# Kernel optimization log

Measured on AMD Instinct MI355X. Metric: run time of the kernel, lower is better.

## Reference

```python
import jax, jax.numpy as jnp
import numpy as np

B = 8192
COND_DIM = 64
OUT_DIM = 64      # output_dim (joint velocity dim)
ACT_DIM = 8       # action_dim (latent action dim)
H1, H2 = 256, 256


def setup_inputs() -> dict:
    key = jax.random.key(0)
    ks = jax.random.split(key, 8)
    inp = {
        "cond_inp": jax.random.normal(ks[0], (B, COND_DIM), dtype=jnp.float32),
        "low_level_action": jax.random.normal(ks[1], (B, OUT_DIM), dtype=jnp.float32),
        # MLP params: cond_dim -> 256 -> 256 -> action_dim*output_dim
        "W1": jax.random.normal(ks[2], (COND_DIM, H1), dtype=jnp.float32) / np.sqrt(COND_DIM),
        "b1": jnp.zeros((H1,), dtype=jnp.float32),
        "W2": jax.random.normal(ks[3], (H1, H2), dtype=jnp.float32) / np.sqrt(H1),
        "b2": jnp.zeros((H2,), dtype=jnp.float32),
        "W3": jax.random.normal(ks[4], (H2, ACT_DIM * OUT_DIM), dtype=jnp.float32) / np.sqrt(H2),
        "b3": jnp.zeros((ACT_DIM * OUT_DIM,), dtype=jnp.float32),
    }
    return inp


def _householder(Hcols):
    # Hcols: [B, n, k]; chain of k batched Householder reflections.
    n = Hcols.shape[1]
    k = Hcols.shape[2]
    I = jnp.eye(n, dtype=Hcols.dtype)
    Q = jnp.broadcast_to(I, (Hcols.shape[0], n, n))
    for c in range(k):  # small fixed unroll over latent action columns
        v = Hcols[:, :, c]                                  # [B, n]
        vvT = jnp.einsum('bi,bj->bij', v, v)                # [B, n, n]
        vTv = jnp.einsum('bi,bi->b', v, v)[:, None, None]   # [B, 1, 1]
        Qi = I - 2.0 * vvT / vTv
        Q = jnp.matmul(Qi, Q)
    return Q[:, :, :k]


def reference(cond_inp, low_level_action, W1, b1, W2, b2, W3, b3):
    # MLP h(cond_inp)
    x = jnp.tanh(cond_inp @ W1 + b1)
    x = jnp.tanh(x @ W2 + b2)
    x = x @ W3 + b3                                    # [B, act*out]
    Hcols = x.reshape(-1, OUT_DIM, ACT_DIM)            # [B, out, act]
    scl_map = _householder(Hcols)                      # [B, out, act], orthonormal cols
    # best action: a* = S^T qdot ; reconstruction: qdot_hat = S a*
    a_star = jnp.einsum('bnk,bn->bk', scl_map, low_level_action)   # [B, act]
    q_dot_hat = jnp.einsum('bnk,bk->bn', scl_map, a_star)          # [B, out]
    return q_dot_hat[..., None]                        # [B, out, 1] (matches tf.matmul shape)
```

## Files before the change

### kernel.cpp

```cpp
#include <hip/hip_runtime.h>

typedef float f4 __attribute__((ext_vector_type(4)));
typedef float f32x4 __attribute__((ext_vector_type(4)));
typedef _Float16 f16x8 __attribute__((ext_vector_type(8)));

#define HSWZ16(o) ((o) ^ (((o) >> 3) & 0x70))

#define BARLG() asm volatile("s_waitcnt lgkmcnt(0)\n\ts_barrier" ::: "memory")

__global__ __launch_bounds__(256) void prep_frags_all(
    const float* __restrict__ W1, const float* __restrict__ W2,
    const float* __restrict__ W3, _Float16* __restrict__ dst) {
    __shared__ float s[32 * 264];
    const int b = blockIdx.x, tid = threadIdx.x;
    const float* W; int N, kt, nh, KT; size_t off;
    if (b < 2)       { W = W1; N = 256; KT = 2; kt = b;            nh = 0;          off = 0; }
    else if (b < 10) { W = W2; N = 256; KT = 8; kt = b - 2;        nh = 0;          off = 16384; }
    else             { W = W3; N = 512; KT = 8; kt = (b - 10) >> 1; nh = (b - 10) & 1; off = 81920; }
    #pragma unroll
    for (int rep = 0; rep < 8; ++rep) {
        int fi = rep * 256 + tid;
        int row = fi >> 6, c4 = fi & 63;
        f4 v = *(const f4*)&W[(kt * 32 + row) * N + nh * 256 + c4 * 4];
        *(f4*)&s[row * 264 + c4 * 4] = v;
    }
    __syncthreads();
    const int wv = tid >> 6, l = tid & 63, lr = l & 15, lg = l >> 4;
    #pragma unroll
    for (int p = 0; p < 4; ++p) {
        int lnt = wv * 4 + p;
        f16x8 o;
        #pragma unroll
        for (int j = 0; j < 8; ++j)
            o[j] = (_Float16)s[(lg * 8 + j) * 264 + lnt * 16 + lr];
        int page = (nh * 16 + lnt) * KT + kt;
        *(f16x8*)&dst[off + (size_t)page * 512 + l * 8] = o;
    }
}

__device__ __forceinline__ float ftanh(float x) {
    float e = __expf(2.0f * x);
    return 1.0f - 2.0f / (e + 1.0f);
}
__device__ __forceinline__ float red8(float x) {
    x += __shfl_xor(x, 1); x += __shfl_xor(x, 2); x += __shfl_xor(x, 4);
    return x;
}

__global__ __launch_bounds__(1024, 4) void scl_mfma(
    const float* __restrict__ cond, const float* __restrict__ act,
    const float* __restrict__ b1, const float* __restrict__ b2,
    const float* __restrict__ b3,
    const _Float16* __restrict__ wf,
    float* __restrict__ out)
{
    __shared__ char smem[33792];
    _Float16* x1 = (_Float16*)smem;
    _Float16* x2 = (_Float16*)(smem + 16896);

    const int tid = threadIdx.x;
    const int w   = tid >> 6;
    const int l   = tid & 63;
    const int lr  = l & 15;
    const int lg  = l >> 4;
    const int rb  = blockIdx.x * 32;
    const f16x8* wp = (const f16x8*)wf;

    f16x8 a1[2][2];
    #pragma unroll
    for (int m = 0; m < 2; ++m) {
        const float* crow = cond + (rb + m * 16 + lr) * 64 + lg * 8;
        #pragma unroll
        for (int kt = 0; kt < 2; ++kt) {
            f4 va = *(const f4*)(crow + kt * 32);
            f4 vb = *(const f4*)(crow + kt * 32 + 4);
            #pragma unroll
            for (int j = 0; j < 4; ++j) {
                a1[m][kt][j]     = (_Float16)va[j];
                a1[m][kt][4 + j] = (_Float16)vb[j];
            }
        }
    }
    f16x8 w1f[2];
    #pragma unroll
    for (int kt = 0; kt < 2; ++kt) w1f[kt] = wp[(w * 2 + kt) * 64 + l];
    f16x8 w2f[8];
    #pragma unroll
    for (int kt = 0; kt < 8; ++kt) w2f[kt] = wp[2048 + (w * 8 + kt) * 64 + l];
    float b1v = b1[w * 16 + lr];
    float b2v = b2[w * 16 + lr];
    float b3v[2];
    #pragma unroll
    for (int n = 0; n < 2; ++n) b3v[n] = b3[(w * 2 + n) * 16 + lr];

    f4 av0 = {}, av1 = {};
    if (w < 4) {
        const float* ap = act + (rb + w * 8 + (l >> 3)) * 64 + (l & 7) * 8;
        av0 = *(const f4*)ap;
        av1 = *(const f4*)(ap + 4);
    }

    {
        f32x4 acc[2] = {};
        #pragma unroll
        for (int kt = 0; kt < 2; ++kt)
            #pragma unroll
            for (int m = 0; m < 2; ++m)
                acc[m] = __builtin_amdgcn_mfma_f32_16x16x32_f16(a1[m][kt], w1f[kt], acc[m], 0, 0, 0);
        #pragma unroll
        for (int m = 0; m < 2; ++m)
            #pragma unroll
            for (int r = 0; r < 4; ++r) {
                float v = ftanh(acc[m][r] + b1v);
                x1[(m * 16 + lg * 4 + r) * 264 + w * 16 + lr] = (_Float16)v;
            }
    }
    BARLG();

    f16x8 w3a[2][4];
    #pragma unroll
    for (int n = 0; n < 2; ++n)
        #pragma unroll
        for (int kt = 0; kt < 4; ++kt)
            w3a[n][kt] = wp[10240 + ((w * 2 + n) * 8 + kt) * 64 + l];
    {
        f32x4 acc[2] = {};
        #pragma unroll
        for (int kt = 0; kt < 8; ++kt) {
            int cb = kt * 32 + lg * 8;
            f16x8 am0 = *(const f16x8*)&x1[lr * 264 + cb];
            f16x8 am1 = *(const f16x8*)&x1[(16 + lr) * 264 + cb];
            acc[0] = __builtin_amdgcn_mfma_f32_16x16x32_f16(am0, w2f[kt], acc[0], 0, 0, 0);
            acc[1] = __builtin_amdgcn_mfma_f32_16x16x32_f16(am1, w2f[kt], acc[1], 0, 0, 0);
        }
        #pragma unroll
        for (int m = 0; m < 2; ++m)
            #pragma unroll
            for (int r = 0; r < 4; ++r) {
                float v = ftanh(acc[m][r] + b2v);
                x2[(m * 16 + lg * 4 + r) * 264 + w * 16 + lr] = (_Float16)v;
            }
    }
    BARLG();

    f16x8 w3b[2][4];
    #pragma unroll
    for (int n = 0; n < 2; ++n)
        #pragma unroll
        for (int kt = 0; kt < 4; ++kt)
            w3b[n][kt] = wp[10240 + ((w * 2 + n) * 8 + (kt + 4)) * 64 + l];
    f32x4 acc3[2][2] = {};
    #pragma unroll
    for (int kt = 0; kt < 4; ++kt) {
        int cb = kt * 32 + lg * 8;
        f16x8 am0 = *(const f16x8*)&x2[lr * 264 + cb];
        f16x8 am1 = *(const f16x8*)&x2[(16 + lr) * 264 + cb];
        #pragma unroll
        for (int n = 0; n < 2; ++n) {
            acc3[0][n] = __builtin_amdgcn_mfma_f32_16x16x32_f16(am0, w3a[n][kt], acc3[0][n], 0, 0, 0);
            acc3[1][n] = __builtin_amdgcn_mfma_f32_16x16x32_f16(am1, w3a[n][kt], acc3[1][n], 0, 0, 0);
        }
    }
    #pragma unroll
    for (int kt = 4; kt < 8; ++kt) {
        int cb = kt * 32 + lg * 8;
        f16x8 am0 = *(const f16x8*)&x2[lr * 264 + cb];
        f16x8 am1 = *(const f16x8*)&x2[(16 + lr) * 264 + cb];
        #pragma unroll
        for (int n = 0; n < 2; ++n) {
            acc3[0][n] = __builtin_amdgcn_mfma_f32_16x16x32_f16(am0, w3b[n][kt - 4], acc3[0][n], 0, 0, 0);
            acc3[1][n] = __builtin_amdgcn_mfma_f32_16x16x32_f16(am1, w3b[n][kt - 4], acc3[1][n], 0, 0, 0);
        }
    }
    BARLG();

    #pragma unroll
    for (int n = 0; n < 2; ++n) {
        int col = (w * 2 + n) * 16 + lr;
        #pragma unroll
        for (int m = 0; m < 2; ++m)
            #pragma unroll
            for (int r = 0; r < 4; ++r) {
                int row = m * 16 + lg * 4 + r;
                *(_Float16*)(smem + row * 1056 + HSWZ16(col * 2)) =
                    (_Float16)(acc3[m][n][r] + b3v[n]);
            }
    }
    BARLG();

    if (w < 4) {
        const int c = l & 7;
        const int hrow = w * 8 + (l >> 3);
        const int grow = rb + hrow;
        f16x8 hv[8];
        #pragma unroll
        for (int j = 0; j < 8; ++j)
            hv[j] = *(const f16x8*)(smem + hrow * 1056 + HSWZ16((c * 8 + j) * 16));
        float h[8][8];
        #pragma unroll
        for (int cc = 0; cc < 8; ++cc)
            #pragma unroll
            for (int j = 0; j < 8; ++j)
                h[cc][j] = (float)hv[j][cc];
        float inv[8];
        #pragma unroll
        for (int cc = 0; cc < 8; ++cc) {
            float s = 0.0f;
            #pragma unroll
            for (int j = 0; j < 8; ++j) s += h[cc][j] * h[cc][j];
            inv[cc] = 2.0f / red8(s);
        }
        float u[8] = {av0[0], av0[1], av0[2], av0[3], av1[0], av1[1], av1[2], av1[3]};
        #pragma unroll
        for (int cc = 7; cc >= 0; --cc) {
            float d = 0.0f;
            #pragma unroll
            for (int j = 0; j < 8; ++j) d += h[cc][j] * u[j];
            float t = inv[cc] * red8(d);
            #pragma unroll
            for (int j = 0; j < 8; ++j) u[j] -= t * h[cc][j];
        }
        float wv[8];
        #pragma unroll
        for (int j = 0; j < 8; ++j) wv[j] = (c == 0) ? u[j] : 0.0f;
        #pragma unroll
        for (int cc = 0; cc < 8; ++cc) {
            float d = 0.0f;
            #pragma unroll
            for (int j = 0; j < 8; ++j) d += h[cc][j] * wv[j];
            float t = inv[cc] * red8(d);
            #pragma unroll
            for (int j = 0; j < 8; ++j) wv[j] -= t * h[cc][j];
        }
        f4 o0 = {wv[0], wv[1], wv[2], wv[3]};
        f4 o1 = {wv[4], wv[5], wv[6], wv[7]};
        float* op = out + grow * 64 + c * 8;
        *(f4*)op = o0;
        *(f4*)(op + 4) = o1;
    }
}

extern "C" void kernel_launch(void* const* d_in, const int* in_sizes, int n_in,
                              void* d_out, int out_size, void* d_ws, size_t ws_size,
                              hipStream_t stream) {
    const float* cond = (const float*)d_in[0];
    const float* act  = (const float*)d_in[1];
    const float* W1   = (const float*)d_in[2];
    const float* b1   = (const float*)d_in[3];
    const float* W2   = (const float*)d_in[4];
    const float* b2   = (const float*)d_in[5];
    const float* W3   = (const float*)d_in[6];
    const float* b3   = (const float*)d_in[7];
    float* outp = (float*)d_out;

    _Float16* wf = (_Float16*)d_ws;
    prep_frags_all<<<dim3(26), dim3(256), 0, stream>>>(W1, W2, W3, wf);
    scl_mfma<<<dim3(256), dim3(1024), 0, stream>>>(cond, act, b1, b2, b3, wf, outp);
}
```

Measured before the change: 25.51 us.

## Restructure MLP into single-wave blocks computing transposed GEMMs over all output tiles

Replaces the 1024-thread, 32-row blocks with 64-thread single-wave blocks that each handle 16 rows. Every wave loops over all output column tiles, with weights as the A operand and activations as the B operand, and folds the bias into the accumulator init. Hidden activations round-trip through swizzled LDS private to the wave, so no barriers are needed. This removes block-wide synchronization and the idle waves in the Householder phase. In exchange, each wave streams the full weight set from global/L2 and only 512 waves run, which may leave the machine underoccupied and bound on weight bandwidth.

```diff
diff --git a/kernel.cpp b/kernel.cpp
--- a/kernel.cpp
+++ b/kernel.cpp
@@ -3,10 +3,14 @@
 typedef float f4 __attribute__((ext_vector_type(4)));
 typedef float f32x4 __attribute__((ext_vector_type(4)));
 typedef _Float16 f16x8 __attribute__((ext_vector_type(8)));
-
-#define HSWZ16(o) ((o) ^ (((o) >> 3) & 0x70))
-
-#define BARLG() asm volatile("s_waitcnt lgkmcnt(0)\n\ts_barrier" ::: "memory")
+typedef _Float16 f16x4 __attribute__((ext_vector_type(4)));
+
+__device__ __forceinline__ int XSW(int row, int fb) {
+    return row * 512 + (fb ^ ((row & 7) << 4));
+}
+__device__ __forceinline__ int HBY(int row, int k, int sub) {
+    return row * 1024 + (((k ^ ((k >> 3) & 7) ^ (row & 7)) << 4) + sub);
+}
 
 __global__ __launch_bounds__(256) void prep_frags_all(
     const float* __restrict__ W1, const float* __restrict__ W2,
@@ -47,155 +51,96 @@
     return x;
 }
 
-__global__ __launch_bounds__(1024, 4) void scl_mfma(
+__global__ __launch_bounds__(64, 2) void scl_wave(
     const float* __restrict__ cond, const float* __restrict__ act,
     const float* __restrict__ b1, const float* __restrict__ b2,
     const float* __restrict__ b3,
     const _Float16* __restrict__ wf,
     float* __restrict__ out)
 {
-    __shared__ char smem[33792];
-    _Float16* x1 = (_Float16*)smem;
-    _Float16* x2 = (_Float16*)(smem + 16896);
-
-    const int tid = threadIdx.x;
-    const int w   = tid >> 6;
-    const int l   = tid & 63;
-    const int lr  = l & 15;
-    const int lg  = l >> 4;
-    const int rb  = blockIdx.x * 32;
+    __shared__ char smem[16384];
+
+    const int l  = threadIdx.x;
+    const int lr = l & 15, lg = l >> 4;
+    const int rb = blockIdx.x * 16;
     const f16x8* wp = (const f16x8*)wf;
 
-    f16x8 a1[2][2];
-    #pragma unroll
-    for (int m = 0; m < 2; ++m) {
-        const float* crow = cond + (rb + m * 16 + lr) * 64 + lg * 8;
+    f4 av[2][2];
+    #pragma unroll
+    for (int p = 0; p < 2; ++p) {
+        const float* ap = act + (rb + 8 * p + (l >> 3)) * 64 + (l & 7) * 8;
+        av[p][0] = *(const f4*)ap;
+        av[p][1] = *(const f4*)(ap + 4);
+    }
+    f16x8 bc[2];
+    {
+        const float* crow = cond + (rb + lr) * 64 + lg * 8;
         #pragma unroll
         for (int kt = 0; kt < 2; ++kt) {
             f4 va = *(const f4*)(crow + kt * 32);
             f4 vb = *(const f4*)(crow + kt * 32 + 4);
             #pragma unroll
             for (int j = 0; j < 4; ++j) {
-                a1[m][kt][j]     = (_Float16)va[j];
-                a1[m][kt][4 + j] = (_Float16)vb[j];
+                bc[kt][j]     = (_Float16)va[j];
+                bc[kt][4 + j] = (_Float16)vb[j];
             }
         }
     }
-    f16x8 w1f[2];
-    #pragma unroll
-    for (int kt = 0; kt < 2; ++kt) w1f[kt] = wp[(w * 2 + kt) * 64 + l];
-    f16x8 w2f[8];
-    #pragma unroll
-    for (int kt = 0; kt < 8; ++kt) w2f[kt] = wp[2048 + (w * 8 + kt) * 64 + l];
-    float b1v = b1[w * 16 + lr];
-    float b2v = b2[w * 16 + lr];
-    float b3v[2];
-    #pragma unroll
-    for (int n = 0; n < 2; ++n) b3v[n] = b3[(w * 2 + n) * 16 + lr];
-
-    f4 av0 = {}, av1 = {};
-    if (w < 4) {
-        const float* ap = act + (rb + w * 8 + (l >> 3)) * 64 + (l & 7) * 8;
-        av0 = *(const f4*)ap;
-        av1 = *(const f4*)(ap + 4);
-    }
-
-    {
-        f32x4 acc[2] = {};
+
+    #pragma unroll 4
+    for (int nt = 0; nt < 16; ++nt) {
+        f4 bi = *(const f4*)&b1[nt * 16 + lg * 4];
+        f32x4 acc = {bi[0], bi[1], bi[2], bi[3]};
         #pragma unroll
         for (int kt = 0; kt < 2; ++kt)
-            #pragma unroll
-            for (int m = 0; m < 2; ++m)
-                acc[m] = __builtin_amdgcn_mfma_f32_16x16x32_f16(a1[m][kt], w1f[kt], acc[m], 0, 0, 0);
-        #pragma unroll
-        for (int m = 0; m < 2; ++m)
-            #pragma unroll
-            for (int r = 0; r < 4; ++r) {
-                float v = ftanh(acc[m][r] + b1v);
-                x1[(m * 16 + lg * 4 + r) * 264 + w * 16 + lr] = (_Float16)v;
-            }
-    }
-    BARLG();
-
-    f16x8 w3a[2][4];
-    #pragma unroll
-    for (int n = 0; n < 2; ++n)
-        #pragma unroll
-        for (int kt = 0; kt < 4; ++kt)
-            w3a[n][kt] = wp[10240 + ((w * 2 + n) * 8 + kt) * 64 + l];
-    {
-        f32x4 acc[2] = {};
-        #pragma unroll
-        for (int kt = 0; kt < 8; ++kt) {
-            int cb = kt * 32 + lg * 8;
-            f16x8 am0 = *(const f16x8*)&x1[lr * 264 + cb];
-            f16x8 am1 = *(const f16x8*)&x1[(16 + lr) * 264 + cb];
-            acc[0] = __builtin_amdgcn_mfma_f32_16x16x32_f16(am0, w2f[kt], acc[0], 0, 0, 0);
-            acc[1] = __builtin_amdgcn_mfma_f32_16x16x32_f16(am1, w2f[kt], acc[1], 0, 0, 0);
-        }
-        #pragma unroll
-        for (int m = 0; m < 2; ++m)
-            #pragma unroll
-            for (int r = 0; r < 4; ++r) {
-                float v = ftanh(acc[m][r] + b2v);
-                x2[(m * 16 + lg * 4 + r) * 264 + w * 16 + lr] = (_Float16)v;
-            }
-    }
-    BARLG();
-
-    f16x8 w3b[2][4];
-    #pragma unroll
-    for (int n = 0; n < 2; ++n)
-        #pragma unroll
-        for (int kt = 0; kt < 4; ++kt)
-            w3b[n][kt] = wp[10240 + ((w * 2 + n) * 8 + (kt + 4)) * 64 + l];
-    f32x4 acc3[2][2] = {};
-    #pragma unroll
-    for (int kt = 0; kt < 4; ++kt) {
-        int cb = kt * 32 + lg * 8;
-        f16x8 am0 = *(const f16x8*)&x2[lr * 264 + cb];
-        f16x8 am1 = *(const f16x8*)&x2[(16 + lr) * 264 + cb];
-        #pragma unroll
-        for (int n = 0; n < 2; ++n) {
-            acc3[0][n] = __builtin_amdgcn_mfma_f32_16x16x32_f16(am0, w3a[n][kt], acc3[0][n], 0, 0, 0);
-            acc3[1][n] = __builtin_amdgcn_mfma_f32_16x16x32_f16(am1, w3a[n][kt], acc3[1][n], 0, 0, 0);
-        }
-    }
-    #pragma unroll
-    for (int kt = 4; kt < 8; ++kt) {
-        int cb = kt * 32 + lg * 8;
-        f16x8 am0 = *(const f16x8*)&x2[lr * 264 + cb];
-        f16x8 am1 = *(const f16x8*)&x2[(16 + lr) * 264 + cb];
-        #pragma unroll
-        for (int n = 0; n < 2; ++n) {
-            acc3[0][n] = __builtin_amdgcn_mfma_f32_16x16x32_f16(am0, w3b[n][kt - 4], acc3[0][n], 0, 0, 0);
-            acc3[1][n] = __builtin_amdgcn_mfma_f32_16x16x32_f16(am1, w3b[n][kt - 4], acc3[1][n], 0, 0, 0);
-        }
-    }
-    BARLG();
-
-    #pragma unroll
-    for (int n = 0; n < 2; ++n) {
-        int col = (w * 2 + n) * 16 + lr;
-        #pragma unroll
-        for (int m = 0; m < 2; ++m)
-            #pragma unroll
-            for (int r = 0; r < 4; ++r) {
-                int row = m * 16 + lg * 4 + r;
-                *(_Float16*)(smem + row * 1056 + HSWZ16(col * 2)) =
-                    (_Float16)(acc3[m][n][r] + b3v[n]);
-            }
-    }
-    BARLG();
-
-    if (w < 4) {
-        const int c = l & 7;
-        const int hrow = w * 8 + (l >> 3);
-        const int grow = rb + hrow;
+            acc = __builtin_amdgcn_mfma_f32_16x16x32_f16(wp[(nt * 2 + kt) * 64 + l], bc[kt], acc, 0, 0, 0);
+        f16x4 hp;
+        #pragma unroll
+        for (int r = 0; r < 4; ++r) hp[r] = (_Float16)ftanh(acc[r]);
+        *(f16x4*)(smem + XSW(lr, (nt * 16 + lg * 4) * 2)) = hp;
+    }
+
+    f16x8 xf[8];
+    #pragma unroll
+    for (int kt = 0; kt < 8; ++kt)
+        xf[kt] = *(const f16x8*)(smem + XSW(lr, (kt * 32 + lg * 8) * 2));
+    #pragma unroll 2
+    for (int nt = 0; nt < 16; ++nt) {
+        f4 bi = *(const f4*)&b2[nt * 16 + lg * 4];
+        f32x4 acc = {bi[0], bi[1], bi[2], bi[3]};
+        #pragma unroll
+        for (int kt = 0; kt < 8; ++kt)
+            acc = __builtin_amdgcn_mfma_f32_16x16x32_f16(wp[2048 + (nt * 8 + kt) * 64 + l], xf[kt], acc, 0, 0, 0);
+        f16x4 hp;
+        #pragma unroll
+        for (int r = 0; r < 4; ++r) hp[r] = (_Float16)ftanh(acc[r]);
+        *(f16x4*)(smem + XSW(lr, (nt * 16 + lg * 4) * 2)) = hp;
+    }
+
+    f16x8 yf[8];
+    #pragma unroll
+    for (int kt = 0; kt < 8; ++kt)
+        yf[kt] = *(const f16x8*)(smem + XSW(lr, (kt * 32 + lg * 8) * 2));
+    #pragma unroll 2
+    for (int nt = 0; nt < 32; ++nt) {
+        f4 bi = *(const f4*)&b3[nt * 16 + lg * 4];
+        f32x4 acc = {bi[0], bi[1], bi[2], bi[3]};
+        #pragma unroll
+        for (int kt = 0; kt < 8; ++kt)
+            acc = __builtin_amdgcn_mfma_f32_16x16x32_f16(wp[10240 + (nt * 8 + kt) * 64 + l], yf[kt], acc, 0, 0, 0);
+        f16x4 hp;
+        #pragma unroll
+        for (int r = 0; r < 4; ++r) hp[r] = (_Float16)acc[r];
+        *(f16x4*)(smem + HBY(lr, 2 * nt + (lg >> 1), 8 * (lg & 1))) = hp;
+    }
+
+    #pragma unroll
+    for (int p = 0; p < 2; ++p) {
+        const int c = l & 7, br = 8 * p + (l >> 3);
         f16x8 hv[8];
         #pragma unroll
         for (int j = 0; j < 8; ++j)
-            hv[j] = *(const f16x8*)(smem + hrow * 1056 + HSWZ16((c * 8 + j) * 16));
+            hv[j] = *(const f16x8*)(smem + HBY(br, 8 * c + j, 0));
         float h[8][8];
         #pragma unroll
         for (int cc = 0; cc < 8; ++cc)
@@ -210,7 +155,8 @@
             for (int j = 0; j < 8; ++j) s += h[cc][j] * h[cc][j];
             inv[cc] = 2.0f / red8(s);
         }
-        float u[8] = {av0[0], av0[1], av0[2], av0[3], av1[0], av1[1], av1[2], av1[3]};
+        float u[8] = {av[p][0][0], av[p][0][1], av[p][0][2], av[p][0][3],
+                      av[p][1][0], av[p][1][1], av[p][1][2], av[p][1][3]};
         #pragma unroll
         for (int cc = 7; cc >= 0; --cc) {
             float d = 0.0f;
@@ -232,9 +178,9 @@
             #pragma unroll
             for (int j = 0; j < 8; ++j) wv[j] -= t * h[cc][j];
         }
+        float* op = out + (rb + br) * 64 + c * 8;
         f4 o0 = {wv[0], wv[1], wv[2], wv[3]};
         f4 o1 = {wv[4], wv[5], wv[6], wv[7]};
-        float* op = out + grow * 64 + c * 8;
         *(f4*)op = o0;
         *(f4*)(op + 4) = o1;
     }
@@ -255,5 +201,5 @@
 
     _Float16* wf = (_Float16*)d_ws;
     prep_frags_all<<<dim3(26), dim3(256), 0, stream>>>(W1, W2, W3, wf);
-    scl_mfma<<<dim3(256), dim3(1024), 0, stream>>>(cond, act, b1, b2, b3, wf, outp);
-}
+    scl_wave<<<dim3(512), dim3(64), 0, stream>>>(cond, act, b1, b2, b3, wf, outp);
+}
```

After: 62.07 us. 2.43x slower.

## Drop weight-prep kernel; load fp32 weight fragments directly in main kernel

Applied to the files above, without the earlier changes.

Removes the separate prep kernel that converted the weights to fp16 MFMA fragment layout. The main kernel now gathers and converts fragments straight from the fp32 weight matrices using strided scalar loads. The point is to save one kernel launch and its serial dependency. The cost is that 256 blocks each do uncoalesced strided fp32 loads, which multiplies weight traffic, though that traffic is mostly L2-resident. Biases are also folded into the accumulator initial values instead of being added after the MFMAs.

```diff
diff --git a/kernel.cpp b/kernel.cpp
--- a/kernel.cpp
+++ b/kernel.cpp
@@ -1,42 +1,13 @@
 #include <hip/hip_runtime.h>
 
 typedef float f4 __attribute__((ext_vector_type(4)));
+typedef float f2 __attribute__((ext_vector_type(2)));
 typedef float f32x4 __attribute__((ext_vector_type(4)));
 typedef _Float16 f16x8 __attribute__((ext_vector_type(8)));
 
 #define HSWZ16(o) ((o) ^ (((o) >> 3) & 0x70))
 
 #define BARLG() asm volatile("s_waitcnt lgkmcnt(0)\n\ts_barrier" ::: "memory")
-
-__global__ __launch_bounds__(256) void prep_frags_all(
-    const float* __restrict__ W1, const float* __restrict__ W2,
-    const float* __restrict__ W3, _Float16* __restrict__ dst) {
-    __shared__ float s[32 * 264];
-    const int b = blockIdx.x, tid = threadIdx.x;
-    const float* W; int N, kt, nh, KT; size_t off;
-    if (b < 2)       { W = W1; N = 256; KT = 2; kt = b;            nh = 0;          off = 0; }
-    else if (b < 10) { W = W2; N = 256; KT = 8; kt = b - 2;        nh = 0;          off = 16384; }
-    else             { W = W3; N = 512; KT = 8; kt = (b - 10) >> 1; nh = (b - 10) & 1; off = 81920; }
-    #pragma unroll
-    for (int rep = 0; rep < 8; ++rep) {
-        int fi = rep * 256 + tid;
-        int row = fi >> 6, c4 = fi & 63;
-        f4 v = *(const f4*)&W[(kt * 32 + row) * N + nh * 256 + c4 * 4];
-        *(f4*)&s[row * 264 + c4 * 4] = v;
-    }
-    __syncthreads();
-    const int wv = tid >> 6, l = tid & 63, lr = l & 15, lg = l >> 4;
-    #pragma unroll
-    for (int p = 0; p < 4; ++p) {
-        int lnt = wv * 4 + p;
-        f16x8 o;
-        #pragma unroll
-        for (int j = 0; j < 8; ++j)
-            o[j] = (_Float16)s[(lg * 8 + j) * 264 + lnt * 16 + lr];
-        int page = (nh * 16 + lnt) * KT + kt;
-        *(f16x8*)&dst[off + (size_t)page * 512 + l * 8] = o;
-    }
-}
 
 __device__ __forceinline__ float ftanh(float x) {
     float e = __expf(2.0f * x);
@@ -47,11 +18,21 @@
     return x;
 }
 
+template<int N>
+__device__ __forceinline__ f16x8 ldfrag(const float* __restrict__ W,
+                                        int kt, int nt, int l) {
+    const float* p = W + (size_t)(kt * 32 + ((l >> 4) << 3)) * N + nt * 16 + (l & 15);
+    f16x8 o;
+    #pragma unroll
+    for (int j = 0; j < 8; ++j) o[j] = (_Float16)p[j * N];
+    return o;
+}
+
 __global__ __launch_bounds__(1024, 4) void scl_mfma(
     const float* __restrict__ cond, const float* __restrict__ act,
-    const float* __restrict__ b1, const float* __restrict__ b2,
-    const float* __restrict__ b3,
-    const _Float16* __restrict__ wf,
+    const float* __restrict__ W1, const float* __restrict__ b1,
+    const float* __restrict__ W2, const float* __restrict__ b2,
+    const float* __restrict__ W3, const float* __restrict__ b3,
     float* __restrict__ out)
 {
     __shared__ char smem[33792];
@@ -64,7 +45,6 @@
     const int lr  = l & 15;
     const int lg  = l >> 4;
     const int rb  = blockIdx.x * 32;
-    const f16x8* wp = (const f16x8*)wf;
 
     f16x8 a1[2][2];
     #pragma unroll
@@ -83,10 +63,10 @@
     }
     f16x8 w1f[2];
     #pragma unroll
-    for (int kt = 0; kt < 2; ++kt) w1f[kt] = wp[(w * 2 + kt) * 64 + l];
+    for (int kt = 0; kt < 2; ++kt) w1f[kt] = ldfrag<256>(W1, kt, w, l);
     f16x8 w2f[8];
     #pragma unroll
-    for (int kt = 0; kt < 8; ++kt) w2f[kt] = wp[2048 + (w * 8 + kt) * 64 + l];
+    for (int kt = 0; kt < 8; ++kt) w2f[kt] = ldfrag<256>(W2, kt, w, l);
     float b1v = b1[w * 16 + lr];
     float b2v = b2[w * 16 + lr];
     float b3v[2];
@@ -101,7 +81,7 @@
     }
 
     {
-        f32x4 acc[2] = {};
+        f32x4 acc[2] = {{b1v, b1v, b1v, b1v}, {b1v, b1v, b1v, b1v}};
         #pragma unroll
         for (int kt = 0; kt < 2; ++kt)
             #pragma unroll
@@ -111,7 +91,7 @@
         for (int m = 0; m < 2; ++m)
             #pragma unroll
             for (int r = 0; r < 4; ++r) {
-                float v = ftanh(acc[m][r] + b1v);
+                float v = ftanh(acc[m][r]);
                 x1[(m * 16 + lg * 4 + r) * 264 + w * 16 + lr] = (_Float16)v;
             }
     }
@@ -122,9 +102,9 @@
     for (int n = 0; n < 2; ++n)
         #pragma unroll
         for (int kt = 0; kt < 4; ++kt)
-            w3a[n][kt] = wp[10240 + ((w * 2 + n) * 8 + kt) * 64 + l];
+            w3a[n][kt] = ldfrag<512>(W3, kt, w * 2 + n, l);
     {
-        f32x4 acc[2] = {};
+        f32x4 acc[2] = {{b2v, b2v, b2v, b2v}, {b2v, b2v, b2v, b2v}};
         #pragma unroll
         for (int kt = 0; kt < 8; ++kt) {
             int cb = kt * 32 + lg * 8;
@@ -137,7 +117,7 @@
         for (int m = 0; m < 2; ++m)
             #pragma unroll
             for (int r = 0; r < 4; ++r) {
-                float v = ftanh(acc[m][r] + b2v);
+                float v = ftanh(acc[m][r]);
                 x2[(m * 16 + lg * 4 + r) * 264 + w * 16 + lr] = (_Float16)v;
             }
     }
@@ -148,8 +128,9 @@
     for (int n = 0; n < 2; ++n)
         #pragma unroll
         for (int kt = 0; kt < 4; ++kt)
-            w3b[n][kt] = wp[10240 + ((w * 2 + n) * 8 + (kt + 4)) * 64 + l];
-    f32x4 acc3[2][2] = {};
+            w3b[n][kt] = ldfrag<512>(W3, kt + 4, w * 2 + n, l);
+    f32x4 acc3[2][2] = {{{b3v[0], b3v[0], b3v[0], b3v[0]}, {b3v[1], b3v[1], b3v[1], b3v[1]}},
+                        {{b3v[0], b3v[0], b3v[0], b3v[0]}, {b3v[1], b3v[1], b3v[1], b3v[1]}}};
     #pragma unroll
     for (int kt = 0; kt < 4; ++kt) {
         int cb = kt * 32 + lg * 8;
@@ -183,7 +164,7 @@
             for (int r = 0; r < 4; ++r) {
                 int row = m * 16 + lg * 4 + r;
                 *(_Float16*)(smem + row * 1056 + HSWZ16(col * 2)) =
-                    (_Float16)(acc3[m][n][r] + b3v[n]);
+                    (_Float16)acc3[m][n][r];
             }
     }
     BARLG();
@@ -253,7 +234,6 @@
     const float* b3   = (const float*)d_in[7];
     float* outp = (float*)d_out;
 
-    _Float16* wf = (_Float16*)d_ws;
-    prep_frags_all<<<dim3(26), dim3(256), 0, stream>>>(W1, W2, W3, wf);
-    scl_mfma<<<dim3(256), dim3(1024), 0, stream>>>(cond, act, b1, b2, b3, wf, outp);
-}
+    scl_mfma<<<dim3(256), dim3(1024), 0, stream>>>(
+        cond, act, W1, b1, W2, b2, W3, b3, outp);
+}
```

Measured after the change: 34.45 us. +35.1%, slower.
